# Kernel optimization log

Measured on AMD Instinct MI355X. Metric: run time of the kernel, lower is better.

## Reference

```python
import jax, jax.numpy as jnp
import numpy as np

D_MODEL = 1024
N_HEADS = 16
HEAD_DIM = D_MODEL // N_HEADS
ROPE_BASE = 10000.0


def rotate_half(x):
    d = x.shape[-1]
    x1, x2 = x[..., : d // 2], x[..., d // 2 :]
    return jnp.concatenate((-x2, x1), axis=-1)


def rope_cos_sin(T, dim, dtype):
    inv_freq = 1.0 / (ROPE_BASE ** (jnp.arange(0, dim, 2, dtype=jnp.float32) / dim))
    t = jnp.arange(T, dtype=jnp.float32)
    freqs = jnp.einsum('i,j->ij', t, inv_freq)  # (T, dim//2)
    emb = jnp.concatenate((freqs, freqs), axis=-1)  # (T, dim)
    return jnp.cos(emb).astype(dtype), jnp.sin(emb).astype(dtype)


def setup_inputs() -> dict:
    key = jax.random.key(0)
    ks = jax.random.split(key, 9)
    s = 0.02
    return {
        'x': jax.random.normal(ks[0], (4, 2048, D_MODEL), dtype=jnp.float32),
        'Wq': jax.random.normal(ks[1], (D_MODEL, D_MODEL), dtype=jnp.float32) * s,
        'bq': jax.random.normal(ks[2], (D_MODEL,), dtype=jnp.float32) * s,
        'Wk': jax.random.normal(ks[3], (D_MODEL, D_MODEL), dtype=jnp.float32) * s,
        'bk': jax.random.normal(ks[4], (D_MODEL,), dtype=jnp.float32) * s,
        'Wv': jax.random.normal(ks[5], (D_MODEL, D_MODEL), dtype=jnp.float32) * s,
        'bv': jax.random.normal(ks[6], (D_MODEL,), dtype=jnp.float32) * s,
        'Wo': jax.random.normal(ks[7], (D_MODEL, D_MODEL), dtype=jnp.float32) * s,
        'bo': jax.random.normal(ks[8], (D_MODEL,), dtype=jnp.float32) * s,
    }


def reference(x, Wq, bq, Wk, bk, Wv, bv, Wo, bo):
    B, T, D = x.shape
    H, hd = N_HEADS, HEAD_DIM

    def proj(W, b):
        y = jnp.einsum('btd,ed->bte', x, W) + b  # torch Linear: x @ W.T + b
        return y.reshape(B, T, H, hd).transpose(0, 2, 1, 3)  # (B,H,T,hd)

    q = proj(Wq, bq)
    k = proj(Wk, bk)
    v = proj(Wv, bv)

    cos, sin = rope_cos_sin(T, hd, x.dtype)  # (T, hd)
    q = q * cos + rotate_half(q) * sin
    k = k * cos + rotate_half(k) * sin

    scores = jnp.einsum('bhqd,bhkd->bhqk', q, k) / jnp.sqrt(jnp.asarray(hd, x.dtype))
    causal = jnp.tril(jnp.ones((T, T), dtype=bool))
    scores = jnp.where(causal, scores, jnp.asarray(-jnp.inf, x.dtype))
    attn = jax.nn.softmax(scores, axis=-1)  # dropout=0 (eval)
    out = jnp.einsum('bhqk,bhkd->bhqd', attn, v)
    out = out.transpose(0, 2, 1, 3).reshape(B, T, D)
    return jnp.einsum('btd,ed->bte', out, Wo) + bo
```

## Files before the change

kernel.cpp:

```cpp
#include <hip/hip_runtime.h>
#include <math.h>

typedef unsigned short u16;
typedef unsigned int u32;
typedef __attribute__((ext_vector_type(4))) float f32x4;
typedef __attribute__((ext_vector_type(8))) __bf16 bf16x8;
typedef __attribute__((ext_vector_type(2))) __bf16 bf16x2;
typedef __attribute__((ext_vector_type(2))) u32 u32x2;

#define B_ 4
#define T_ 2048
#define D_ 1024
#define H_ 16
#define HD_ 64

__device__ __forceinline__ u16 f2b_rne(float f) {
  u32 u = __float_as_uint(f);
  u32 r = (u + 0x7FFFu + ((u >> 16) & 1u)) >> 16;
  return (u16)r;
}
__device__ __forceinline__ float b2f(u16 u) {
  return __uint_as_float(((u32)u) << 16);
}
__device__ __forceinline__ u32 pack2(float a, float b) {
  bf16x2 v = {(__bf16)a, (__bf16)b};
  return __builtin_bit_cast(u32, v);
}
__device__ __forceinline__ void gload_lds16(const void* g, void* l) {
  __builtin_amdgcn_global_load_lds(
      (const __attribute__((address_space(1))) u32*)g,
      (__attribute__((address_space(3))) u32*)l, 16, 0, 0);
}

__global__ void f2b4_kernel(const float* __restrict__ in, u16* __restrict__ out, int n4) {
  int i = blockIdx.x * 256 + threadIdx.x;
  if (i < n4) {
    f32x4 v = ((const f32x4*)in)[i];
    u32x2 o;
    o.x = pack2(v[0], v[1]);
    o.y = pack2(v[2], v[3]);
    ((u32x2*)out)[i] = o;
  }
}

__global__ void rope_qk_kernel(const u16* __restrict__ qkv,
                               u16* __restrict__ Q, u16* __restrict__ K) {
  int j = blockIdx.x * 256 + threadIdx.x;
  if (j >= (B_ * T_) * (D_ / 2)) return;
  int row = j >> 9;
  int p = j & 511;
  int h = p >> 5, i = p & 31;
  int b = row >> 11, t = row & (T_ - 1);
  const u16* base = qkv + (size_t)row * (3 * D_);
  float inv_freq = exp2f(-(float)i * 0.4152410118609203f);
  float ang = (float)t * inv_freq;
  float s, c;
  sincosf(ang, &s, &c);
  int qi = h * HD_ + i;
  float q1 = b2f(base[qi]),      q2 = b2f(base[qi + 32]);
  float k1 = b2f(base[D_ + qi]), k2 = b2f(base[D_ + qi + 32]);
  float qo1 = (q1 * c - q2 * s) * 0.125f;
  float qo2 = (q2 * c + q1 * s) * 0.125f;
  float ko1 = k1 * c - k2 * s;
  float ko2 = k2 * c + k1 * s;
  size_t bh = (size_t)(b * H_ + h);
  size_t qk = bh * T_ * HD_ + (size_t)t * HD_ + i;
  Q[qk]      = f2b_rne(qo1);
  Q[qk + 32] = f2b_rne(qo2);
  K[qk]      = f2b_rne(ko1);
  K[qk + 32] = f2b_rne(ko2);
}

__global__ __launch_bounds__(256) void vt_kernel(const u16* __restrict__ qkv,
                                                 u16* __restrict__ VT) {
  __shared__ __align__(16) u16 tile[64 * 64];
  const int x = blockIdx.x;
  const int bh = blockIdx.y;
  const int b = bh >> 4, h = bh & 15;
  const int tid = threadIdx.x;
  const u16* src = qkv + (size_t)(b * T_ + x * 64) * (3 * D_) + 2 * D_ + h * HD_;
#pragma unroll
  for (int it = 0; it < 2; ++it) {
    int r = it * 32 + (tid >> 3);
    int chunk = tid & 7;
    bf16x8 v = *(const bf16x8*)(src + (size_t)r * (3 * D_) + chunk * 8);
    u16 tmp[8];
    *(bf16x8*)tmp = v;
#pragma unroll
    for (int jj = 0; jj < 8; ++jj) {
      int i = chunk * 8 + jj;
      int byte = i * 128 + ((2 * r) ^ ((i >> 3) << 4));
      *(u16*)((char*)tile + byte) = tmp[jj];
    }
  }
  __syncthreads();
  const int i = tid >> 2, tc = tid & 3;
  u16* dst = VT + (size_t)bh * HD_ * T_ + (size_t)i * T_ + x * 64 + tc * 16;
#pragma unroll
  for (int half = 0; half < 2; ++half) {
    int byte = i * 128 + ((tc * 32 + half * 16) ^ ((i >> 3) << 4));
    *(bf16x8*)(dst + half * 8) = *(const bf16x8*)((char*)tile + byte);
  }
}

template <bool F32OUT>
__global__ __launch_bounds__(256) void gemm_bt_kernel(
    const u16* __restrict__ A, const u16* __restrict__ Bm,
    const float* __restrict__ bias, void* __restrict__ Cout,
    int M, int N, int K) {
  __shared__ __align__(16) u16 As[128 * 64];
  __shared__ __align__(16) u16 Bs[128 * 64];
  const int tid = threadIdx.x;
  const int wid = tid >> 6, lane = tid & 63;
  const int l15 = lane & 15, lhi = lane >> 4;
  const int brow = blockIdx.x, bcol = blockIdx.y;
  const int wr = wid >> 1, wc = wid & 1;

  f32x4 acc[4][4] = {};

  for (int k0 = 0; k0 < K; k0 += 64) {
#pragma unroll
    for (int cc = 0; cc < 4; cc++) {
      int chunk = cc * 4 + wid;
      int slot = chunk * 64 + lane;
      int row = slot >> 3;
      int colb = (slot & 7) << 4;
      gload_lds16((const char*)(A + (size_t)(brow * 128 + row) * K + k0) + colb,
                  (char*)As + chunk * 1024);
      gload_lds16((const char*)(Bm + (size_t)(bcol * 128 + row) * K + k0) + colb,
                  (char*)Bs + chunk * 1024);
    }
    __syncthreads();
#pragma unroll
    for (int kk = 0; kk < 2; kk++) {
      bf16x8 af[4], bfr[4];
#pragma unroll
      for (int i = 0; i < 4; i++)
        af[i] = *(const bf16x8*)&As[(wr * 64 + i * 16 + l15) * 64 + kk * 32 + lhi * 8];
#pragma unroll
      for (int j = 0; j < 4; j++)
        bfr[j] = *(const bf16x8*)&Bs[(wc * 64 + j * 16 + l15) * 64 + kk * 32 + lhi * 8];
#pragma unroll
      for (int i = 0; i < 4; i++)
#pragma unroll
        for (int j = 0; j < 4; j++)
          acc[i][j] = __builtin_amdgcn_mfma_f32_16x16x32_bf16(af[i], bfr[j], acc[i][j], 0, 0, 0);
    }
    __syncthreads();
  }
#pragma unroll
  for (int i = 0; i < 4; i++)
#pragma unroll
    for (int r = 0; r < 4; r++) {
      int row = brow * 128 + wr * 64 + i * 16 + lhi * 4 + r;
#pragma unroll
      for (int j = 0; j < 4; j++) {
        int col = bcol * 128 + wc * 64 + j * 16 + l15;
        float v = acc[i][j][r] + bias[col];
        if (F32OUT)
          ((float*)Cout)[(size_t)row * N + col] = v;
        else
          ((u16*)Cout)[(size_t)row * N + col] = f2b_rne(v);
      }
    }
}

__global__ __launch_bounds__(256) void attn_kernel(
    const u16* __restrict__ Q, const u16* __restrict__ K,
    const u16* __restrict__ VT, u16* __restrict__ O) {
  __shared__ __align__(16) u16 Plds[4][2][16 * 64];
  const int tid = threadIdx.x;
  const int w = tid >> 6, lane = tid & 63;
  const int l15 = lane & 15, lhi = lane >> 4;
  const int bid = blockIdx.x;
  const int xq = 15 - (bid >> 6);
  const int bh = bid & 63;
  const int q0 = xq * 128;
  const int bb = bh >> 4, hh = bh & 15;

  const u16* Qb = Q + (size_t)bh * T_ * HD_;
  const u16* Kb = K + (size_t)bh * T_ * HD_;
  const u16* Vb = VT + (size_t)bh * HD_ * T_;

  const int qbase = q0 + w * 32;

  bf16x8 qf[2][2];
#pragma unroll
  for (int g = 0; g < 2; ++g) {
    const u16* qr = Qb + (size_t)(qbase + g * 16 + l15) * HD_ + lhi * 8;
    qf[g][0] = *(const bf16x8*)(qr);
    qf[g][1] = *(const bf16x8*)(qr + 32);
  }

  float mrun[2] = {-1e30f, -1e30f}, lrun[2] = {0.f, 0.f};
  f32x4 oacc[2][4] = {};

  const int nb = (qbase + 95) >> 6;
  const int sw = (l15 & 7) << 4;

  for (int t = 0; t < nb; ++t) {
    const int t0 = t * 64;

    f32x4 s[2][4];
    const u16* Kt = Kb + (size_t)t0 * HD_;
#pragma unroll
    for (int ks = 0; ks < 4; ++ks) {
      const u16* kr = Kt + (size_t)(ks * 16 + l15) * HD_ + lhi * 8;
      bf16x8 kf0 = *(const bf16x8*)(kr);
      bf16x8 kf1 = *(const bf16x8*)(kr + 32);
#pragma unroll
      for (int g = 0; g < 2; ++g) {
        f32x4 z = {0.f, 0.f, 0.f, 0.f};
        z = __builtin_amdgcn_mfma_f32_16x16x32_bf16(kf0, qf[g][0], z, 0, 0, 0);
        s[g][ks] = __builtin_amdgcn_mfma_f32_16x16x32_bf16(kf1, qf[g][1], z, 0, 0, 0);
      }
    }

    bf16x8 vf[4][2];
#pragma unroll
    for (int db = 0; db < 4; ++db) {
      const u16* vr = Vb + (size_t)(db * 16 + l15) * T_ + t0 + lhi * 8;
      vf[db][0] = *(const bf16x8*)(vr);
      vf[db][1] = *(const bf16x8*)(vr + 32);
    }

    if (t == nb - 1) {
#pragma unroll
      for (int g = 0; g < 2; ++g) {
        int qr = qbase + g * 16 + l15;
#pragma unroll
        for (int ks = 0; ks < 4; ++ks)
#pragma unroll
          for (int r = 0; r < 4; ++r)
            if (t0 + ks * 16 + lhi * 4 + r > qr) s[g][ks][r] = -1e30f;
      }
    }

#pragma unroll
    for (int g = 0; g < 2; ++g) {
      float mx = s[g][0][0];
#pragma unroll
      for (int ks = 0; ks < 4; ++ks)
#pragma unroll
        for (int r = 0; r < 4; ++r) mx = fmaxf(mx, s[g][ks][r]);
      mx = fmaxf(mx, __shfl_xor(mx, 16));
      mx = fmaxf(mx, __shfl_xor(mx, 32));
      float mnew = fmaxf(mrun[g], mx);
      float corr = __expf(mrun[g] - mnew);
      mrun[g] = mnew;
      float rs = 0.f;
      char* prow = (char*)&Plds[w][g][0] + l15 * 128;
#pragma unroll
      for (int ks = 0; ks < 4; ++ks) {
        float e0 = __expf(s[g][ks][0] - mnew);
        float e1 = __expf(s[g][ks][1] - mnew);
        float e2 = __expf(s[g][ks][2] - mnew);
        float e3 = __expf(s[g][ks][3] - mnew);
        rs += (e0 + e1) + (e2 + e3);
        u32x2 pw;
        pw.x = pack2(e0, e1);
        pw.y = pack2(e2, e3);
        *(u32x2*)(prow + ((ks * 32 + lhi * 8) ^ sw)) = pw;
      }
      rs += __shfl_xor(rs, 16);
      rs += __shfl_xor(rs, 32);
      lrun[g] = lrun[g] * corr + rs;
#pragma unroll
      for (int db = 0; db < 4; ++db)
#pragma unroll
        for (int r = 0; r < 4; ++r) oacc[g][db][r] *= corr;
    }

#pragma unroll
    for (int g = 0; g < 2; ++g) {
      const char* prow = (const char*)&Plds[w][g][0] + l15 * 128;
#pragma unroll
      for (int c = 0; c < 2; ++c) {
        bf16x8 pb = *(const bf16x8*)(prow + ((c * 64 + lhi * 16) ^ sw));
#pragma unroll
        for (int db = 0; db < 4; ++db)
          oacc[g][db] = __builtin_amdgcn_mfma_f32_16x16x32_bf16(vf[db][c], pb, oacc[g][db], 0, 0, 0);
      }
    }
  }

#pragma unroll
  for (int g = 0; g < 2; ++g) {
    float invl = 1.0f / lrun[g];
    int qr = qbase + g * 16 + l15;
    u16* orow = O + ((size_t)bb * T_ + qr) * D_ + hh * HD_ + lhi * 4;
#pragma unroll
    for (int db = 0; db < 4; ++db) {
      u32x2 wv;
      wv.x = pack2(oacc[g][db][0] * invl, oacc[g][db][1] * invl);
      wv.y = pack2(oacc[g][db][2] * invl, oacc[g][db][3] * invl);
      *(u32x2*)(orow + db * 16) = wv;
    }
  }
}

extern "C" void kernel_launch(void* const* d_in, const int* in_sizes, int n_in,
                              void* d_out, int out_size, void* d_ws, size_t ws_size,
                              hipStream_t stream) {
  const float* x  = (const float*)d_in[0];
  const float* Wq = (const float*)d_in[1];
  const float* bq = (const float*)d_in[2];
  const float* Wk = (const float*)d_in[3];
  const float* bk = (const float*)d_in[4];
  const float* Wv = (const float*)d_in[5];
  const float* bv = (const float*)d_in[6];
  const float* Wo = (const float*)d_in[7];
  const float* bo = (const float*)d_in[8];

  char* ws = (char*)d_ws;
  u16*  XB    = (u16*)(ws + 0);
  u16*  QKV   = (u16*)(ws + 16777216);
  u16*  Qb    = (u16*)(ws + 67108864);
  u16*  Kb    = (u16*)(ws + 83886080);
  u16*  VTb   = (u16*)(ws + 100663296);
  u16*  WQKVB = (u16*)(ws + 117440512);
  u16*  WOB   = (u16*)(ws + 123731968);
  float* BQKV = (float*)(ws + 125829120);
  u16*  ATTO  = XB;

  hipMemcpyAsync(BQKV,        bq, D_ * 4, hipMemcpyDeviceToDevice, stream);
  hipMemcpyAsync(BQKV + D_,   bk, D_ * 4, hipMemcpyDeviceToDevice, stream);
  hipMemcpyAsync(BQKV + 2*D_, bv, D_ * 4, hipMemcpyDeviceToDevice, stream);

  f2b4_kernel<<<8192, 256, 0, stream>>>(x, XB, B_ * T_ * D_ / 4);
  f2b4_kernel<<<1024, 256, 0, stream>>>(Wq, WQKVB,               D_ * D_ / 4);
  f2b4_kernel<<<1024, 256, 0, stream>>>(Wk, WQKVB + D_ * D_,     D_ * D_ / 4);
  f2b4_kernel<<<1024, 256, 0, stream>>>(Wv, WQKVB + 2 * D_ * D_, D_ * D_ / 4);
  f2b4_kernel<<<1024, 256, 0, stream>>>(Wo, WOB,                 D_ * D_ / 4);

  gemm_bt_kernel<false><<<dim3(64, 24), 256, 0, stream>>>(
      XB, WQKVB, BQKV, QKV, B_ * T_, 3 * D_, D_);

  rope_qk_kernel<<<16384, 256, 0, stream>>>(QKV, Qb, Kb);
  vt_kernel<<<dim3(T_ / 64, B_ * H_), 256, 0, stream>>>(QKV, VTb);

  attn_kernel<<<1024, 256, 0, stream>>>(Qb, Kb, VTb, ATTO);

  gemm_bt_kernel<true><<<dim3(64, 8), 256, 0, stream>>>(
      ATTO, WOB, bo, d_out, B_ * T_, D_, D_);

  (void)in_sizes; (void)n_in; (void)out_size; (void)ws_size;
}
```

Before: 280.1 us.

## Rebalance causal attention work, use exp2 softmax with lazy rescale, fuse weight casts

Attention now uses 128-thread blocks in which each wave handles one 16-row query strip from the front and its mirror strip from the back, so every wave does a similar amount of causal work. Softmax folds log2(e) into the Q scale so it can use exp2f, and it skips rescaling the accumulator unless the running max grows by more than a threshold. The four weight-cast launches are merged into one kernel, and the GEMM remaps block indices so neighbouring blocks share tiles in cache. The trade-offs are fewer rows per wave, which reduces K/V reuse, and extra divergence and bookkeeping from the lazy-rescale check.

Result: slower. 389.4 us (+39.0%).

```diff
diff --git a/kernel.cpp b/kernel.cpp
--- a/kernel.cpp
+++ b/kernel.cpp
@@ -41,6 +41,20 @@
     o.y = pack2(v[2], v[3]);
     ((u32x2*)out)[i] = o;
   }
+}
+
+__global__ void f2bw_kernel(const float* __restrict__ Wq, const float* __restrict__ Wk,
+                            const float* __restrict__ Wv, const float* __restrict__ Wo,
+                            u16* __restrict__ wqkv, u16* __restrict__ wo) {
+  int sel = blockIdx.x >> 10;
+  int i = (blockIdx.x & 1023) * 256 + threadIdx.x;
+  const float* src = sel == 0 ? Wq : sel == 1 ? Wk : sel == 2 ? Wv : Wo;
+  u16* dst = sel < 3 ? wqkv + (size_t)sel * (D_ * D_) : wo;
+  f32x4 v = ((const f32x4*)src)[i];
+  u32x2 o;
+  o.x = pack2(v[0], v[1]);
+  o.y = pack2(v[2], v[3]);
+  ((u32x2*)dst)[i] = o;
 }
 
 __global__ void rope_qk_kernel(const u16* __restrict__ qkv,
@@ -59,8 +73,9 @@
   int qi = h * HD_ + i;
   float q1 = b2f(base[qi]),      q2 = b2f(base[qi + 32]);
   float k1 = b2f(base[D_ + qi]), k2 = b2f(base[D_ + qi + 32]);
-  float qo1 = (q1 * c - q2 * s) * 0.125f;
-  float qo2 = (q2 * c + q1 * s) * 0.125f;
+  const float QS = 0.18033688011f;
+  float qo1 = (q1 * c - q2 * s) * QS;
+  float qo2 = (q2 * c + q1 * s) * QS;
   float ko1 = k1 * c - k2 * s;
   float ko2 = k2 * c + k1 * s;
   size_t bh = (size_t)(b * H_ + h);
@@ -113,7 +128,12 @@
   const int tid = threadIdx.x;
   const int wid = tid >> 6, lane = tid & 63;
   const int l15 = lane & 15, lhi = lane >> 4;
-  const int brow = blockIdx.x, bcol = blockIdx.y;
+  const int NY = gridDim.y;
+  int lin = blockIdx.y * 64 + blockIdx.x;
+  int qq = (NY << 6) >> 3;
+  int swz = (lin & 7) * qq + (lin >> 3);
+  const int brow = swz / NY;
+  const int bcol = swz - brow * NY;
   const int wr = wid >> 1, wc = wid & 1;
 
   f32x4 acc[4][4] = {};
@@ -165,97 +185,84 @@
     }
 }
 
-__global__ __launch_bounds__(256) void attn_kernel(
+__global__ __launch_bounds__(128, 4) void attn_kernel(
     const u16* __restrict__ Q, const u16* __restrict__ K,
     const u16* __restrict__ VT, u16* __restrict__ O) {
-  __shared__ __align__(16) u16 Plds[4][2][16 * 64];
+  __shared__ __align__(16) u16 Plds[2][16 * 64];
   const int tid = threadIdx.x;
   const int w = tid >> 6, lane = tid & 63;
   const int l15 = lane & 15, lhi = lane >> 4;
-  const int bid = blockIdx.x;
-  const int xq = 15 - (bid >> 6);
-  const int bh = bid & 63;
-  const int q0 = xq * 128;
+  const int task = ((blockIdx.x >> 3) << 1) | w;
+  const int bh = ((blockIdx.x & 7) << 3) | (task & 7);
+  const int a = task >> 3;
   const int bb = bh >> 4, hh = bh & 15;
 
   const u16* Qb = Q + (size_t)bh * T_ * HD_;
   const u16* Kb = K + (size_t)bh * T_ * HD_;
   const u16* Vb = VT + (size_t)bh * HD_ * T_;
-
-  const int qbase = q0 + w * 32;
-
-  bf16x8 qf[2][2];
-#pragma unroll
-  for (int g = 0; g < 2; ++g) {
-    const u16* qr = Qb + (size_t)(qbase + g * 16 + l15) * HD_ + lhi * 8;
-    qf[g][0] = *(const bf16x8*)(qr);
-    qf[g][1] = *(const bf16x8*)(qr + 32);
-  }
-
-  float mrun[2] = {-1e30f, -1e30f}, lrun[2] = {0.f, 0.f};
-  f32x4 oacc[2][4] = {};
-
-  const int nb = (qbase + 95) >> 6;
   const int sw = (l15 & 7) << 4;
-
-  for (int t = 0; t < nb; ++t) {
-    const int t0 = t * 64;
-
-    f32x4 s[2][4];
-    const u16* Kt = Kb + (size_t)t0 * HD_;
-#pragma unroll
-    for (int ks = 0; ks < 4; ++ks) {
-      const u16* kr = Kt + (size_t)(ks * 16 + l15) * HD_ + lhi * 8;
-      bf16x8 kf0 = *(const bf16x8*)(kr);
-      bf16x8 kf1 = *(const bf16x8*)(kr + 32);
-#pragma unroll
-      for (int g = 0; g < 2; ++g) {
+  char* prow = (char*)&Plds[w][0] + l15 * 128;
+
+  for (int seg = 0; seg < 2; ++seg) {
+    const int sg = seg ? (127 - a) : a;
+    const int qrow = sg * 16 + l15;
+    const u16* qr = Qb + (size_t)qrow * HD_ + lhi * 8;
+    const bf16x8 qf0 = *(const bf16x8*)(qr);
+    const bf16x8 qf1 = *(const bf16x8*)(qr + 32);
+    float mrun = -1e30f, lrun = 0.f;
+    f32x4 oacc[4] = {};
+    const int nb = (sg >> 2) + 1;
+
+    for (int t = 0; t < nb; ++t) {
+      const int t0 = t * 64;
+      f32x4 s[4];
+#pragma unroll
+      for (int ks = 0; ks < 4; ++ks) {
+        const u16* kr = Kb + (size_t)(t0 + ks * 16 + l15) * HD_ + lhi * 8;
+        bf16x8 kf0 = *(const bf16x8*)(kr);
+        bf16x8 kf1 = *(const bf16x8*)(kr + 32);
         f32x4 z = {0.f, 0.f, 0.f, 0.f};
-        z = __builtin_amdgcn_mfma_f32_16x16x32_bf16(kf0, qf[g][0], z, 0, 0, 0);
-        s[g][ks] = __builtin_amdgcn_mfma_f32_16x16x32_bf16(kf1, qf[g][1], z, 0, 0, 0);
-      }
-    }
-
-    bf16x8 vf[4][2];
-#pragma unroll
-    for (int db = 0; db < 4; ++db) {
-      const u16* vr = Vb + (size_t)(db * 16 + l15) * T_ + t0 + lhi * 8;
-      vf[db][0] = *(const bf16x8*)(vr);
-      vf[db][1] = *(const bf16x8*)(vr + 32);
-    }
-
-    if (t == nb - 1) {
-#pragma unroll
-      for (int g = 0; g < 2; ++g) {
-        int qr = qbase + g * 16 + l15;
+        z = __builtin_amdgcn_mfma_f32_16x16x32_bf16(kf0, qf0, z, 0, 0, 0);
+        s[ks] = __builtin_amdgcn_mfma_f32_16x16x32_bf16(kf1, qf1, z, 0, 0, 0);
+      }
+      bf16x8 vf[4][2];
+#pragma unroll
+      for (int db = 0; db < 4; ++db) {
+        const u16* vr = Vb + (size_t)(db * 16 + l15) * T_ + t0 + lhi * 8;
+        vf[db][0] = *(const bf16x8*)(vr);
+        vf[db][1] = *(const bf16x8*)(vr + 32);
+      }
+      if (t == nb - 1) {
 #pragma unroll
         for (int ks = 0; ks < 4; ++ks)
 #pragma unroll
           for (int r = 0; r < 4; ++r)
-            if (t0 + ks * 16 + lhi * 4 + r > qr) s[g][ks][r] = -1e30f;
-      }
-    }
-
-#pragma unroll
-    for (int g = 0; g < 2; ++g) {
-      float mx = s[g][0][0];
+            if (t0 + ks * 16 + lhi * 4 + r > qrow) s[ks][r] = -1e30f;
+      }
+      float mx = s[0][0];
 #pragma unroll
       for (int ks = 0; ks < 4; ++ks)
 #pragma unroll
-        for (int r = 0; r < 4; ++r) mx = fmaxf(mx, s[g][ks][r]);
+        for (int r = 0; r < 4; ++r) mx = fmaxf(mx, s[ks][r]);
       mx = fmaxf(mx, __shfl_xor(mx, 16));
       mx = fmaxf(mx, __shfl_xor(mx, 32));
-      float mnew = fmaxf(mrun[g], mx);
-      float corr = __expf(mrun[g] - mnew);
-      mrun[g] = mnew;
+      if (!__all(mx <= mrun + 8.f)) {
+        float mnew = fmaxf(mrun, mx);
+        float corr = exp2f(mrun - mnew);
+        lrun *= corr;
+#pragma unroll
+        for (int db = 0; db < 4; ++db)
+#pragma unroll
+          for (int r = 0; r < 4; ++r) oacc[db][r] *= corr;
+        mrun = mnew;
+      }
       float rs = 0.f;
-      char* prow = (char*)&Plds[w][g][0] + l15 * 128;
 #pragma unroll
       for (int ks = 0; ks < 4; ++ks) {
-        float e0 = __expf(s[g][ks][0] - mnew);
-        float e1 = __expf(s[g][ks][1] - mnew);
-        float e2 = __expf(s[g][ks][2] - mnew);
-        float e3 = __expf(s[g][ks][3] - mnew);
+        float e0 = exp2f(s[ks][0] - mrun);
+        float e1 = exp2f(s[ks][1] - mrun);
+        float e2 = exp2f(s[ks][2] - mrun);
+        float e3 = exp2f(s[ks][3] - mrun);
         rs += (e0 + e1) + (e2 + e3);
         u32x2 pw;
         pw.x = pack2(e0, e1);
@@ -264,36 +271,22 @@
       }
       rs += __shfl_xor(rs, 16);
       rs += __shfl_xor(rs, 32);
-      lrun[g] = lrun[g] * corr + rs;
-#pragma unroll
-      for (int db = 0; db < 4; ++db)
-#pragma unroll
-        for (int r = 0; r < 4; ++r) oacc[g][db][r] *= corr;
-    }
-
-#pragma unroll
-    for (int g = 0; g < 2; ++g) {
-      const char* prow = (const char*)&Plds[w][g][0] + l15 * 128;
+      lrun += rs;
 #pragma unroll
       for (int c = 0; c < 2; ++c) {
         bf16x8 pb = *(const bf16x8*)(prow + ((c * 64 + lhi * 16) ^ sw));
 #pragma unroll
         for (int db = 0; db < 4; ++db)
-          oacc[g][db] = __builtin_amdgcn_mfma_f32_16x16x32_bf16(vf[db][c], pb, oacc[g][db], 0, 0, 0);
-      }
-    }
-  }
-
-#pragma unroll
-  for (int g = 0; g < 2; ++g) {
-    float invl = 1.0f / lrun[g];
-    int qr = qbase + g * 16 + l15;
-    u16* orow = O + ((size_t)bb * T_ + qr) * D_ + hh * HD_ + lhi * 4;
+          oacc[db] = __builtin_amdgcn_mfma_f32_16x16x32_bf16(vf[db][c], pb, oacc[db], 0, 0, 0);
+      }
+    }
+    float invl = 1.0f / lrun;
+    u16* orow = O + ((size_t)bb * T_ + qrow) * D_ + hh * HD_ + lhi * 4;
 #pragma unroll
     for (int db = 0; db < 4; ++db) {
       u32x2 wv;
-      wv.x = pack2(oacc[g][db][0] * invl, oacc[g][db][1] * invl);
-      wv.y = pack2(oacc[g][db][2] * invl, oacc[g][db][3] * invl);
+      wv.x = pack2(oacc[db][0] * invl, oacc[db][1] * invl);
+      wv.y = pack2(oacc[db][2] * invl, oacc[db][3] * invl);
       *(u32x2*)(orow + db * 16) = wv;
     }
   }
@@ -328,10 +321,7 @@
   hipMemcpyAsync(BQKV + 2*D_, bv, D_ * 4, hipMemcpyDeviceToDevice, stream);
 
   f2b4_kernel<<<8192, 256, 0, stream>>>(x, XB, B_ * T_ * D_ / 4);
-  f2b4_kernel<<<1024, 256, 0, stream>>>(Wq, WQKVB,               D_ * D_ / 4);
-  f2b4_kernel<<<1024, 256, 0, stream>>>(Wk, WQKVB + D_ * D_,     D_ * D_ / 4);
-  f2b4_kernel<<<1024, 256, 0, stream>>>(Wv, WQKVB + 2 * D_ * D_, D_ * D_ / 4);
-  f2b4_kernel<<<1024, 256, 0, stream>>>(Wo, WOB,                 D_ * D_ / 4);
+  f2bw_kernel<<<4096, 256, 0, stream>>>(Wq, Wk, Wv, Wo, WQKVB, WOB);
 
   gemm_bt_kernel<false><<<dim3(64, 24), 256, 0, stream>>>(
       XB, WQKVB, BQKV, QKV, B_ * T_, 3 * D_, D_);
@@ -339,7 +329,7 @@
   rope_qk_kernel<<<16384, 256, 0, stream>>>(QKV, Qb, Kb);
   vt_kernel<<<dim3(T_ / 64, B_ * H_), 256, 0, stream>>>(QKV, VTb);
 
-  attn_kernel<<<1024, 256, 0, stream>>>(Qb, Kb, VTb, ATTO);
+  attn_kernel<<<2048, 128, 0, stream>>>(Qb, Kb, VTb, ATTO);
 
   gemm_bt_kernel<true><<<dim3(64, 8), 256, 0, stream>>>(
       ATTO, WOB, bo, d_out, B_ * T_, D_, D_);
```

## Balance causal attention work, skip softmax rescales, swizzle GEMM blocks, merge weight casts

Applied to the files above, without the earlier changes.

The attention kernel now pairs a short query tile with its mirrored long tile in each wave, so every block does similar causal work. Blocks are mapped so that each XCD serves a fixed set of heads. It folds log2(e) into the Q scale so the softmax can use exp2f, and it skips the running-max rescale while the new max stays within a threshold of the old one. The GEMM remaps block indices so neighbouring blocks share data in cache, and the four weight-cast launches become one launch. Together these target tail imbalance, launch overhead, cache misses and redundant rescale work, at the cost of more complex indexing and a lazy rescale that could overflow if scores jump sharply.

After: 334.6 us. +19.5%, slower.

```diff
diff --git a/kernel.cpp b/kernel.cpp
--- a/kernel.cpp
+++ b/kernel.cpp
@@ -41,6 +41,20 @@
     o.y = pack2(v[2], v[3]);
     ((u32x2*)out)[i] = o;
   }
+}
+
+__global__ void f2bw_kernel(const float* __restrict__ Wq, const float* __restrict__ Wk,
+                            const float* __restrict__ Wv, const float* __restrict__ Wo,
+                            u16* __restrict__ wqkv, u16* __restrict__ wo) {
+  int sel = blockIdx.x >> 10;
+  int i = (blockIdx.x & 1023) * 256 + threadIdx.x;
+  const float* src = sel == 0 ? Wq : sel == 1 ? Wk : sel == 2 ? Wv : Wo;
+  u16* dst = sel < 3 ? wqkv + (size_t)sel * (D_ * D_) : wo;
+  f32x4 v = ((const f32x4*)src)[i];
+  u32x2 o;
+  o.x = pack2(v[0], v[1]);
+  o.y = pack2(v[2], v[3]);
+  ((u32x2*)dst)[i] = o;
 }
 
 __global__ void rope_qk_kernel(const u16* __restrict__ qkv,
@@ -59,8 +73,9 @@
   int qi = h * HD_ + i;
   float q1 = b2f(base[qi]),      q2 = b2f(base[qi + 32]);
   float k1 = b2f(base[D_ + qi]), k2 = b2f(base[D_ + qi + 32]);
-  float qo1 = (q1 * c - q2 * s) * 0.125f;
-  float qo2 = (q2 * c + q1 * s) * 0.125f;
+  const float QS = 0.18033688011f;
+  float qo1 = (q1 * c - q2 * s) * QS;
+  float qo2 = (q2 * c + q1 * s) * QS;
   float ko1 = k1 * c - k2 * s;
   float ko2 = k2 * c + k1 * s;
   size_t bh = (size_t)(b * H_ + h);
@@ -113,7 +128,12 @@
   const int tid = threadIdx.x;
   const int wid = tid >> 6, lane = tid & 63;
   const int l15 = lane & 15, lhi = lane >> 4;
-  const int brow = blockIdx.x, bcol = blockIdx.y;
+  const int NY = gridDim.y;
+  int lin = blockIdx.y * 64 + blockIdx.x;
+  int qq = (NY << 6) >> 3;
+  int swz = (lin & 7) * qq + (lin >> 3);
+  const int brow = swz / NY;
+  const int bcol = swz - brow * NY;
   const int wr = wid >> 1, wc = wid & 1;
 
   f32x4 acc[4][4] = {};
@@ -172,22 +192,24 @@
   const int tid = threadIdx.x;
   const int w = tid >> 6, lane = tid & 63;
   const int l15 = lane & 15, lhi = lane >> 4;
-  const int bid = blockIdx.x;
-  const int xq = 15 - (bid >> 6);
-  const int bh = bid & 63;
-  const int q0 = xq * 128;
+  const int xcd = blockIdx.x & 7;
+  const int j = blockIdx.x >> 3;
+  const int bh = (xcd << 3) | (j & 7);
+  const int a = ((j >> 3) << 2) | w;
   const int bb = bh >> 4, hh = bh & 15;
 
   const u16* Qb = Q + (size_t)bh * T_ * HD_;
   const u16* Kb = K + (size_t)bh * T_ * HD_;
   const u16* Vb = VT + (size_t)bh * HD_ * T_;
-
-  const int qbase = q0 + w * 32;
+  const int sw = (l15 & 7) << 4;
+
+  const int qrw[2] = {a * 16 + l15, (127 - a) * 16 + l15};
+  const int nbg[2] = {(a >> 2) + 1, ((127 - a) >> 2) + 1};
 
   bf16x8 qf[2][2];
 #pragma unroll
   for (int g = 0; g < 2; ++g) {
-    const u16* qr = Qb + (size_t)(qbase + g * 16 + l15) * HD_ + lhi * 8;
+    const u16* qr = Qb + (size_t)qrw[g] * HD_ + lhi * 8;
     qf[g][0] = *(const bf16x8*)(qr);
     qf[g][1] = *(const bf16x8*)(qr + 32);
   }
@@ -195,17 +217,13 @@
   float mrun[2] = {-1e30f, -1e30f}, lrun[2] = {0.f, 0.f};
   f32x4 oacc[2][4] = {};
 
-  const int nb = (qbase + 95) >> 6;
-  const int sw = (l15 & 7) << 4;
-
-  for (int t = 0; t < nb; ++t) {
+  for (int t = 0; t < nbg[1]; ++t) {
     const int t0 = t * 64;
 
     f32x4 s[2][4];
-    const u16* Kt = Kb + (size_t)t0 * HD_;
 #pragma unroll
     for (int ks = 0; ks < 4; ++ks) {
-      const u16* kr = Kt + (size_t)(ks * 16 + l15) * HD_ + lhi * 8;
+      const u16* kr = Kb + (size_t)(t0 + ks * 16 + l15) * HD_ + lhi * 8;
       bf16x8 kf0 = *(const bf16x8*)(kr);
       bf16x8 kf1 = *(const bf16x8*)(kr + 32);
 #pragma unroll
@@ -224,20 +242,16 @@
       vf[db][1] = *(const bf16x8*)(vr + 32);
     }
 
-    if (t == nb - 1) {
-#pragma unroll
-      for (int g = 0; g < 2; ++g) {
-        int qr = qbase + g * 16 + l15;
+#pragma unroll
+    for (int g = 1; g >= 0; --g) {
+      if (g == 0 && t >= nbg[0]) break;
+      if (t == nbg[g] - 1) {
 #pragma unroll
         for (int ks = 0; ks < 4; ++ks)
 #pragma unroll
           for (int r = 0; r < 4; ++r)
-            if (t0 + ks * 16 + lhi * 4 + r > qr) s[g][ks][r] = -1e30f;
-      }
-    }
-
-#pragma unroll
-    for (int g = 0; g < 2; ++g) {
+            if (t0 + ks * 16 + lhi * 4 + r > qrw[g]) s[g][ks][r] = -1e30f;
+      }
       float mx = s[g][0][0];
 #pragma unroll
       for (int ks = 0; ks < 4; ++ks)
@@ -245,17 +259,24 @@
         for (int r = 0; r < 4; ++r) mx = fmaxf(mx, s[g][ks][r]);
       mx = fmaxf(mx, __shfl_xor(mx, 16));
       mx = fmaxf(mx, __shfl_xor(mx, 32));
-      float mnew = fmaxf(mrun[g], mx);
-      float corr = __expf(mrun[g] - mnew);
-      mrun[g] = mnew;
+      if (!__all(mx <= mrun[g] + 8.f)) {
+        float mnew = fmaxf(mrun[g], mx);
+        float corr = exp2f(mrun[g] - mnew);
+        lrun[g] *= corr;
+#pragma unroll
+        for (int db = 0; db < 4; ++db)
+#pragma unroll
+          for (int r = 0; r < 4; ++r) oacc[g][db][r] *= corr;
+        mrun[g] = mnew;
+      }
+      char* prow = (char*)&Plds[w][g][0] + l15 * 128;
       float rs = 0.f;
-      char* prow = (char*)&Plds[w][g][0] + l15 * 128;
 #pragma unroll
       for (int ks = 0; ks < 4; ++ks) {
-        float e0 = __expf(s[g][ks][0] - mnew);
-        float e1 = __expf(s[g][ks][1] - mnew);
-        float e2 = __expf(s[g][ks][2] - mnew);
-        float e3 = __expf(s[g][ks][3] - mnew);
+        float e0 = exp2f(s[g][ks][0] - mrun[g]);
+        float e1 = exp2f(s[g][ks][1] - mrun[g]);
+        float e2 = exp2f(s[g][ks][2] - mrun[g]);
+        float e3 = exp2f(s[g][ks][3] - mrun[g]);
         rs += (e0 + e1) + (e2 + e3);
         u32x2 pw;
         pw.x = pack2(e0, e1);
@@ -264,16 +285,7 @@
       }
       rs += __shfl_xor(rs, 16);
       rs += __shfl_xor(rs, 32);
-      lrun[g] = lrun[g] * corr + rs;
-#pragma unroll
-      for (int db = 0; db < 4; ++db)
-#pragma unroll
-        for (int r = 0; r < 4; ++r) oacc[g][db][r] *= corr;
-    }
-
-#pragma unroll
-    for (int g = 0; g < 2; ++g) {
-      const char* prow = (const char*)&Plds[w][g][0] + l15 * 128;
+      lrun[g] += rs;
 #pragma unroll
       for (int c = 0; c < 2; ++c) {
         bf16x8 pb = *(const bf16x8*)(prow + ((c * 64 + lhi * 16) ^ sw));
@@ -287,8 +299,7 @@
 #pragma unroll
   for (int g = 0; g < 2; ++g) {
     float invl = 1.0f / lrun[g];
-    int qr = qbase + g * 16 + l15;
-    u16* orow = O + ((size_t)bb * T_ + qr) * D_ + hh * HD_ + lhi * 4;
+    u16* orow = O + ((size_t)bb * T_ + qrw[g]) * D_ + hh * HD_ + lhi * 4;
 #pragma unroll
     for (int db = 0; db < 4; ++db) {
       u32x2 wv;
@@ -328,10 +339,7 @@
   hipMemcpyAsync(BQKV + 2*D_, bv, D_ * 4, hipMemcpyDeviceToDevice, stream);
 
   f2b4_kernel<<<8192, 256, 0, stream>>>(x, XB, B_ * T_ * D_ / 4);
-  f2b4_kernel<<<1024, 256, 0, stream>>>(Wq, WQKVB,               D_ * D_ / 4);
-  f2b4_kernel<<<1024, 256, 0, stream>>>(Wk, WQKVB + D_ * D_,     D_ * D_ / 4);
-  f2b4_kernel<<<1024, 256, 0, stream>>>(Wv, WQKVB + 2 * D_ * D_, D_ * D_ / 4);
-  f2b4_kernel<<<1024, 256, 0, stream>>>(Wo, WOB,                 D_ * D_ / 4);
+  f2bw_kernel<<<4096, 256, 0, stream>>>(Wq, Wk, Wv, Wo, WQKVB, WOB);
 
   gemm_bt_kernel<false><<<dim3(64, 24), 256, 0, stream>>>(
       XB, WQKVB, BQKV, QKV, B_ * T_, 3 * D_, D_);
```
